# Optimization experiments

Hardware: AMD Instinct MI355X
Metric: run time of the kernel (lower is better)

Reference implementation:

```python
import jax, jax.numpy as jnp
import numpy as np

E = 768   # embed_dim
S = 128   # slots
T = 3     # recurrence steps
B = 64    # batch
L = 512   # sequence length of z
LN_EPS = 1e-5


def _layernorm(x, g, b):
    mu = jnp.mean(x, axis=-1, keepdims=True)
    var = jnp.mean((x - mu) ** 2, axis=-1, keepdims=True)
    return (x - mu) / jnp.sqrt(var + LN_EPS) * g + b


def _mha(q, k, v, Wq, bq, Wk, bk, Wv, bv, Wo, bo):
    # single-head MultiheadAttention, batch_first; PyTorch Linear: x @ W.T + b
    Q = q @ Wq.T + bq                     # [B, Lq, E]
    K = k @ Wk.T + bk                     # [B, Lk, E]
    V = v @ Wv.T + bv
    scale = 1.0 / jnp.sqrt(jnp.asarray(Q.shape[-1], Q.dtype))
    scores = jnp.einsum('bqe,bke->bqk', Q, K) * scale
    A = jax.nn.softmax(scores, axis=-1)
    O = jnp.einsum('bqk,bke->bqe', A, V)
    return O @ Wo.T + bo


def _gru_cell(x, h, Wih, bih, Whh, bhh):
    # PyTorch GRUCell gate order: r, z, n
    gi = x @ Wih.T + bih
    gh = h @ Whh.T + bhh
    i_r, i_z, i_n = jnp.split(gi, 3, axis=-1)
    h_r, h_z, h_n = jnp.split(gh, 3, axis=-1)
    r = jax.nn.sigmoid(i_r + h_r)
    zt = jax.nn.sigmoid(i_z + h_z)
    n = jnp.tanh(i_n + r * h_n)
    return (1.0 - zt) * n + zt * h


def setup_inputs() -> dict:
    key = jax.random.key(0)
    ks = jax.random.split(key, 24)
    w = lambda k, shape: jax.random.normal(k, shape, dtype=jnp.float32) * 0.02
    inp = {
        'z': jax.random.normal(ks[0], (B, L, E), dtype=jnp.float32),
        'slots': w(ks[1], (1, S, E)),
        'ln_g': jnp.ones((E,), jnp.float32),
        'ln_b': jnp.zeros((E,), jnp.float32),
        # write attention
        'w_wq': w(ks[2], (E, E)), 'w_bq': jnp.zeros((E,), jnp.float32),
        'w_wk': w(ks[3], (E, E)), 'w_bk': jnp.zeros((E,), jnp.float32),
        'w_wv': w(ks[4], (E, E)), 'w_bv': jnp.zeros((E,), jnp.float32),
        'w_wo': w(ks[5], (E, E)), 'w_bo': jnp.zeros((E,), jnp.float32),
        # read attention
        'r_wq': w(ks[6], (E, E)), 'r_bq': jnp.zeros((E,), jnp.float32),
        'r_wk': w(ks[7], (E, E)), 'r_bk': jnp.zeros((E,), jnp.float32),
        'r_wv': w(ks[8], (E, E)), 'r_bv': jnp.zeros((E,), jnp.float32),
        'r_wo': w(ks[9], (E, E)), 'r_bo': jnp.zeros((E,), jnp.float32),
        # GRUCell
        'gru_wih': w(ks[10], (3 * E, E)), 'gru_bih': jnp.zeros((3 * E,), jnp.float32),
        'gru_whh': w(ks[11], (3 * E, E)), 'gru_bhh': jnp.zeros((3 * E,), jnp.float32),
    }
    return inp


def reference(z, slots, ln_g, ln_b,
              w_wq, w_bq, w_wk, w_bk, w_wv, w_bv, w_wo, w_bo,
              r_wq, r_bq, r_wk, r_bk, r_wv, r_bv, r_wo, r_bo,
              gru_wih, gru_bih, gru_whh, gru_bhh):
    bsz = z.shape[0]
    memory = jnp.broadcast_to(slots, (bsz, S, E))
    for _ in range(T):
        memory = _layernorm(memory, ln_g, ln_b)
        upd = _mha(memory, z, z, w_wq, w_bq, w_wk, w_bk, w_wv, w_bv, w_wo, w_bo)
        memory = _gru_cell(upd.reshape(-1, E), memory.reshape(-1, E),
                           gru_wih, gru_bih, gru_whh, gru_bhh).reshape(bsz, S, E)
    out = _mha(z, memory, memory, r_wq, r_bq, r_wk, r_bk, r_wv, r_bv, r_wo, r_bo)
    return out
```

## Files before the change

kernel.cpp:

```cpp
#include <hip/hip_runtime.h>
#include <hip/hip_bf16.h>
#include <math.h>


typedef __attribute__((ext_vector_type(4))) float f32x4;
typedef __attribute__((ext_vector_type(8))) short short8;
typedef __attribute__((ext_vector_type(4))) unsigned short us4;

__device__ __forceinline__ unsigned short f2bf(float x) {
  union { float f; unsigned u; } v; v.f = x;
  unsigned r = v.u + 0x7fffu + ((v.u >> 16) & 1u);
  return (unsigned short)(r >> 16);
}
__device__ __forceinline__ float bf2f(unsigned short u) {
  union { unsigned u; float f; } v; v.u = (unsigned)u << 16; return v.f;
}

__device__ __forceinline__ void g2l16(const void* g, void* l) {
  __builtin_amdgcn_global_load_lds(
      (const __attribute__((address_space(1))) unsigned int*)g,
      (__attribute__((address_space(3))) unsigned int*)l, 16, 0, 0);
}

__device__ __forceinline__ float wsum(float v) {
#pragma unroll
  for (int o = 32; o > 0; o >>= 1) v += __shfl_xor(v, o, 64);
  return v;
}
__device__ __forceinline__ float wmax(float v) {
#pragma unroll
  for (int o = 32; o > 0; o >>= 1) v = fmaxf(v, __shfl_xor(v, o, 64));
  return v;
}

__device__ __forceinline__ void xcd_map(int& tn, int& tm, long long& bz) {
  const int gx = gridDim.x, gy = gridDim.y, gz = gridDim.z;
  const int nwg = gx * gy * gz;
  const int lin = blockIdx.x + gx * (blockIdx.y + gy * blockIdx.z);
  const int q = nwg >> 3, r = nwg & 7;
  const int xcd = lin & 7, jj = lin >> 3;
  const int w = (xcd < r ? xcd * (q + 1) : r * (q + 1) + (xcd - r) * q) + jj;
  tn = w % gx;
  const int t2 = w / gx;
  tm = t2 % gy;
  bz = t2 / gy;
}

__device__ __forceinline__ void c_write_128(
    void* Cg, size_t cb, int N, int tm, int tn, int wr, int wc, int lane,
    const f32x4 acc[4][4], const float* bias, bool has_bias, float alpha, int omode)
{
#pragma unroll
  for (int a = 0; a < 4; ++a) {
    const int row0 = tm * 128 + wr * 64 + a * 16 + (lane >> 4) * 4;
#pragma unroll
    for (int b = 0; b < 4; ++b) {
      const int col = tn * 128 + wc * 64 + b * 16 + (lane & 15);
      float bv = has_bias ? bias[col] : 0.f;
#pragma unroll
      for (int rr = 0; rr < 4; ++rr) {
        float v = acc[a][b][rr] * alpha + bv;
        if (omode == 0)
          ((float*)Cg)[cb + (size_t)(row0 + rr) * N + col] = v;
        else
          ((unsigned short*)Cg)[cb + (size_t)(row0 + rr) * N + col] = f2bf(v);
      }
    }
  }
}

template<int OMODE, bool BIAS>
__device__ __forceinline__ void gemm_body(
    const unsigned short* __restrict__ A, const unsigned short* __restrict__ B,
    const float* __restrict__ bias, void* __restrict__ Cg, size_t cb,
    int N, int K, int tm, int tn, float alpha,
    unsigned short* As, unsigned short* Bs)
{
  const int tid  = threadIdx.x;
  const int lane = tid & 63;
  const int wv   = tid >> 6;
  const int wr   = wv >> 1, wc = wv & 1;

  A += (size_t)tm * 128 * K;
  B += (size_t)tn * 128 * K;

  const int srow = wv * 16 + (lane >> 2);
  const int kby  = (lane & 3) * 16;

  f32x4 acc[4][4];
#pragma unroll
  for (int a = 0; a < 4; ++a)
#pragma unroll
    for (int b = 0; b < 4; ++b) acc[a][b] = (f32x4)(0.f);

  const int mrow = wr * 64 + (lane & 15);
  const int nrow = wc * 64 + (lane & 15);
  const int koff = (lane >> 4) * 8;

  for (int kt = 0; kt < K; kt += 32) {
#pragma unroll
    for (int i = 0; i < 2; ++i) {
      g2l16((const char*)(A + (size_t)(i * 64 + srow) * K + kt) + kby,
            (char*)As + i * 4096 + wv * 1024);
      g2l16((const char*)(B + (size_t)(i * 64 + srow) * K + kt) + kby,
            (char*)Bs + i * 4096 + wv * 1024);
    }
    __syncthreads();
    short8 af[4], bf[4];
#pragma unroll
    for (int a = 0; a < 4; ++a) af[a] = *(const short8*)&As[(mrow + a * 16) * 32 + koff];
#pragma unroll
    for (int b = 0; b < 4; ++b) bf[b] = *(const short8*)&Bs[(nrow + b * 16) * 32 + koff];
#pragma unroll
    for (int a = 0; a < 4; ++a)
#pragma unroll
      for (int b = 0; b < 4; ++b)
        acc[a][b] = __builtin_amdgcn_mfma_f32_16x16x32_bf16(af[a], bf[b], acc[a][b], 0, 0, 0);
    __syncthreads();
  }
  c_write_128(Cg, cb, N, tm, tn, wr, wc, lane, acc, bias, BIAS, alpha, OMODE);
}

template<int OMODE, bool BIAS>
__global__ __launch_bounds__(256) void gemm_nt64(
    const unsigned short* __restrict__ Ag, const unsigned short* __restrict__ Bg,
    const float* __restrict__ bias, void* __restrict__ Cg,
    int M, int N, int K, long long sA, long long sB, long long sC,
    long long sBias, float alpha)
{
  __shared__ __align__(16) unsigned short As[128 * 64];
  __shared__ __align__(16) unsigned short Bs[128 * 64];

  const int tid  = threadIdx.x;
  const int lane = tid & 63;
  const int wv   = tid >> 6;
  const int wr   = wv >> 1, wc = wv & 1;

  int tn, tm; long long bz;
  xcd_map(tn, tm, bz);

  const unsigned short* A = Ag + bz * sA + (size_t)tm * 128 * K;
  const unsigned short* B = Bg + bz * sB + (size_t)tn * 128 * K;

  auto swz = [](int o) { return o ^ (((o >> 7) & 7) << 4); };

  const char* aSrc[4];
  const char* bSrc[4];
#pragma unroll
  for (int c = 0; c < 4; ++c) {
    const int olog = swz(c * 4096 + tid * 16);
    const int row = olog >> 7, cbyte = olog & 127;
    aSrc[c] = (const char*)(A + (size_t)row * K) + cbyte;
    bSrc[c] = (const char*)(B + (size_t)row * K) + cbyte;
  }
  const int mrow = wr * 64 + (lane & 15);
  const int nrow = wc * 64 + (lane & 15);
  const int kb   = (lane >> 4) * 16;
  int aoff[4][2], boff[4][2];
#pragma unroll
  for (int a = 0; a < 4; ++a)
#pragma unroll
    for (int h = 0; h < 2; ++h) {
      aoff[a][h] = swz((mrow + a * 16) * 128 + h * 64 + kb);
      boff[a][h] = swz((nrow + a * 16) * 128 + h * 64 + kb);
    }

  f32x4 acc[4][4];
#pragma unroll
  for (int a = 0; a < 4; ++a)
#pragma unroll
    for (int b = 0; b < 4; ++b) acc[a][b] = (f32x4)(0.f);

  size_t ktB = 0;
  for (int kt = 0; kt < K; kt += 64, ktB += 128) {
#pragma unroll
    for (int c = 0; c < 4; ++c) {
      g2l16(aSrc[c] + ktB, (char*)As + c * 4096 + wv * 1024);
      g2l16(bSrc[c] + ktB, (char*)Bs + c * 4096 + wv * 1024);
    }
    __syncthreads();
#pragma unroll
    for (int h = 0; h < 2; ++h) {
      short8 af[4], bf[4];
#pragma unroll
      for (int a = 0; a < 4; ++a)
        af[a] = *(const short8*)((char*)As + aoff[a][h]);
#pragma unroll
      for (int b = 0; b < 4; ++b)
        bf[b] = *(const short8*)((char*)Bs + boff[b][h]);
#pragma unroll
      for (int a = 0; a < 4; ++a)
#pragma unroll
        for (int b = 0; b < 4; ++b)
          acc[a][b] = __builtin_amdgcn_mfma_f32_16x16x32_bf16(af[a], bf[b], acc[a][b], 0, 0, 0);
    }
    __syncthreads();
  }

  const float* bp = BIAS ? bias + bz * sBias : (const float*)nullptr;
  c_write_128(Cg, (size_t)(bz * sC), N, tm, tn, wr, wc, lane, acc, bp, BIAS, alpha, OMODE);
}

struct QuadPtrs {
  const unsigned short* a[4];
  const unsigned short* b[4];
  unsigned short* c[4];
};
__global__ __launch_bounds__(256) void gemm_nt_quad(QuadPtrs p) {
  __shared__ __align__(16) unsigned short As[128 * 32];
  __shared__ __align__(16) unsigned short Bs[128 * 32];
  const int zi = blockIdx.z;
  gemm_body<1, false>(p.a[zi], p.b[zi], nullptr, (void*)p.c[zi], 0,
                      768, 768, blockIdx.y, blockIdx.x, 1.0f, As, Bs);
}

__global__ __launch_bounds__(256) void softmax512(
    const float* __restrict__ sc, unsigned short* __restrict__ p)
{
  const int row  = blockIdx.x * 4 + (threadIdx.x >> 6);
  const int lane = threadIdx.x & 63;
  const float4* sr = (const float4*)(sc + (size_t)row * 512);
  float4 v[2];
  float m = -1e30f;
#pragma unroll
  for (int j = 0; j < 2; ++j) {
    v[j] = sr[lane + 64 * j];
    m = fmaxf(m, fmaxf(fmaxf(v[j].x, v[j].y), fmaxf(v[j].z, v[j].w)));
  }
  m = wmax(m);
  float s = 0.f;
#pragma unroll
  for (int j = 0; j < 2; ++j) {
    v[j].x = __expf(v[j].x - m); v[j].y = __expf(v[j].y - m);
    v[j].z = __expf(v[j].z - m); v[j].w = __expf(v[j].w - m);
    s += v[j].x + v[j].y + v[j].z + v[j].w;
  }
  s = wsum(s);
  const float inv = 1.f / s;
  us4* pr = (us4*)(p + (size_t)row * 512);
#pragma unroll
  for (int j = 0; j < 2; ++j) {
    us4 o;
    o.x = f2bf(v[j].x * inv); o.y = f2bf(v[j].y * inv);
    o.z = f2bf(v[j].z * inv); o.w = f2bf(v[j].w * inv);
    pr[lane + 64 * j] = o;
  }
}

__global__ __launch_bounds__(256) void softmax128(
    const float* __restrict__ sc, unsigned short* __restrict__ p)
{
  const int row  = blockIdx.x * 4 + (threadIdx.x >> 6);
  const int lane = threadIdx.x & 63;
  const float* sr = sc + (size_t)row * 128;
  float v[2];
  float m = -1e30f;
#pragma unroll
  for (int j = 0; j < 2; ++j) { v[j] = sr[lane + 64 * j]; m = fmaxf(m, v[j]); }
  m = wmax(m);
  float s = 0.f;
#pragma unroll
  for (int j = 0; j < 2; ++j) { v[j] = __expf(v[j] - m); s += v[j]; }
  s = wsum(s);
  const float inv = 1.f / s;
  unsigned short* pr = p + (size_t)row * 128;
#pragma unroll
  for (int j = 0; j < 2; ++j) pr[lane + 64 * j] = f2bf(v[j] * inv);
}

template<bool GHB, bool EMITLN>
__global__ __launch_bounds__(256) void gru_ln_combine(
    const unsigned short* __restrict__ gi, const unsigned short* __restrict__ gh,
    float* __restrict__ mem, const float* __restrict__ g, const float* __restrict__ b,
    unsigned short* __restrict__ outb)
{
  __shared__ float ps[4], pq[4];
  const size_t row = blockIdx.x;
  const int tid = threadIdx.x, wv = tid >> 6, lane = tid & 63;
  float* mr = mem + row * 768;
  const size_t ghrow = GHB ? (row & 127) : row;
  float v[3];
  float s = 0.f, q = 0.f;
#pragma unroll
  for (int k = 0; k < 3; ++k) {
    v[k] = mr[tid + 256 * k];
    s += v[k]; q += v[k] * v[k];
  }
  s = wsum(s); q = wsum(q);
  if (lane == 0) { ps[wv] = s; pq[wv] = q; }
  __syncthreads();
  s = ps[0] + ps[1] + ps[2] + ps[3];
  q = pq[0] + pq[1] + pq[2] + pq[3];
  const float mu = s * (1.f / 768.f);
  const float rstd = rsqrtf(q * (1.f / 768.f) - mu * mu + 1e-5f);
  float nv[3];
  float s2 = 0.f, q2 = 0.f;
#pragma unroll
  for (int k = 0; k < 3; ++k) {
    const int c = tid + 256 * k;
    const float h = (v[k] - mu) * rstd * g[c] + b[c];
    const float ir  = bf2f(gi[row * 2304 + c]);
    const float iz  = bf2f(gi[row * 2304 + 768 + c]);
    const float in_ = bf2f(gi[row * 2304 + 1536 + c]);
    const float hr  = bf2f(gh[ghrow * 2304 + c]);
    const float hz  = bf2f(gh[ghrow * 2304 + 768 + c]);
    const float hn  = bf2f(gh[ghrow * 2304 + 1536 + c]);
    const float rg = 1.f / (1.f + __expf(-(ir + hr)));
    const float zg = 1.f / (1.f + __expf(-(iz + hz)));
    const float n  = tanhf(in_ + rg * hn);
    nv[k] = (1.f - zg) * n + zg * h;
    mr[c] = nv[k];
    s2 += nv[k]; q2 += nv[k] * nv[k];
  }
  if (EMITLN) {
    s2 = wsum(s2); q2 = wsum(q2);
    __syncthreads();
    if (lane == 0) { ps[wv] = s2; pq[wv] = q2; }
    __syncthreads();
    s2 = ps[0] + ps[1] + ps[2] + ps[3];
    q2 = pq[0] + pq[1] + pq[2] + pq[3];
    const float mu2 = s2 * (1.f / 768.f);
    const float rstd2 = rsqrtf(q2 * (1.f / 768.f) - mu2 * mu2 + 1e-5f);
#pragma unroll
    for (int k = 0; k < 3; ++k) {
      const int c = tid + 256 * k;
      outb[row * 768 + c] = f2bf((nv[k] - mu2) * rstd2 * g[c] + b[c]);
    }
  } else {
#pragma unroll
    for (int k = 0; k < 3; ++k) {
      const int c = tid + 256 * k;
      outb[row * 768 + c] = f2bf(nv[k]);
    }
  }
}

__global__ __launch_bounds__(256) void cvt_weights(
    const float* p0, const float* p1, const float* p2, const float* p3,
    const float* p4, const float* p5, const float* p6, const float* p7,
    const float* p8, const float* p9, unsigned short* __restrict__ dst)
{
  const int i = blockIdx.x * 256 + threadIdx.x;
  if (i >= 2064384) return;
  const float* src; int base;
  if      (i < 147456)  { src = p0; base = 0; }
  else if (i < 294912)  { src = p1; base = 147456; }
  else if (i < 442368)  { src = p2; base = 294912; }
  else if (i < 589824)  { src = p3; base = 442368; }
  else if (i < 737280)  { src = p4; base = 589824; }
  else if (i < 884736)  { src = p5; base = 737280; }
  else if (i < 1032192) { src = p6; base = 884736; }
  else if (i < 1179648) { src = p7; base = 1032192; }
  else if (i < 1622016) { src = p8; base = 1179648; }
  else                  { src = p9; base = 1622016; }
  const float4 v = ((const float4*)src)[i - base];
  us4 o;
  o.x = f2bf(v.x); o.y = f2bf(v.y); o.z = f2bf(v.z); o.w = f2bf(v.w);
  ((us4*)dst)[i] = o;
}

__global__ __launch_bounds__(256) void init_mem(
    const float* __restrict__ slots, const float* __restrict__ g,
    const float* __restrict__ b, float* __restrict__ memf,
    unsigned short* __restrict__ memb)
{
  __shared__ float ps[4], pq[4];
  const int s = blockIdx.x;
  const int g0 = blockIdx.y * 8;
  const int tid = threadIdx.x, wv = tid >> 6, lane = tid & 63;
  const float* sr = slots + (size_t)s * 768;
  float v[3];
  float su = 0.f, qu = 0.f;
#pragma unroll
  for (int k = 0; k < 3; ++k) { v[k] = sr[tid + 256 * k]; su += v[k]; qu += v[k] * v[k]; }
  su = wsum(su); qu = wsum(qu);
  if (lane == 0) { ps[wv] = su; pq[wv] = qu; }
  __syncthreads();
  su = ps[0] + ps[1] + ps[2] + ps[3];
  qu = pq[0] + pq[1] + pq[2] + pq[3];
  const float mu = su * (1.f / 768.f);
  const float rstd = rsqrtf(qu * (1.f / 768.f) - mu * mu + 1e-5f);
  unsigned short lb[3];
#pragma unroll
  for (int k = 0; k < 3; ++k) {
    const int c = tid + 256 * k;
    lb[k] = f2bf((v[k] - mu) * rstd * g[c] + b[c]);
  }
  for (int bb = g0; bb < g0 + 8; ++bb) {
    float* mrow = memf + ((size_t)bb * 128 + s) * 768;
    unsigned short* brow = memb + ((size_t)bb * 128 + s) * 768;
#pragma unroll
    for (int k = 0; k < 3; ++k) { mrow[tid + 256 * k] = v[k]; brow[tid + 256 * k] = lb[k]; }
  }
}

struct TPtrs { const unsigned short* s[6]; unsigned short* d[6]; };
__global__ void transpose_multi(TPtrs p) {
  __shared__ unsigned short t[32][33];
  const unsigned short* in = p.s[blockIdx.z];
  unsigned short* out = p.d[blockIdx.z];
  const int c0 = blockIdx.x * 32, r0 = blockIdx.y * 32;
  const int x = threadIdx.x, y = threadIdx.y;
#pragma unroll
  for (int k = 0; k < 32; k += 8)
    t[y + k][x] = in[(size_t)(r0 + y + k) * 768 + c0 + x];
  __syncthreads();
#pragma unroll
  for (int k = 0; k < 32; k += 8)
    out[(size_t)(c0 + y + k) * 768 + r0 + x] = t[x][y + k];
}

__global__ __launch_bounds__(256) void matvec_row2b(
    const unsigned short* __restrict__ A0, const float* __restrict__ x0,
    float* __restrict__ y0,
    const unsigned short* __restrict__ A1, const float* __restrict__ x1,
    float* __restrict__ y1)
{
  const int task = blockIdx.x / 192;
  const int row = (blockIdx.x % 192) * 4 + (threadIdx.x >> 6);
  const int lane = threadIdx.x & 63;
  const unsigned short* r = (task ? A1 : A0) + (size_t)row * 768;
  const float* x = task ? x1 : x0;
  float s = 0.f;
#pragma unroll
  for (int j = 0; j < 12; ++j) s += bf2f(r[lane + 64 * j]) * x[lane + 64 * j];
  s = wsum(s);
  if (lane == 0) (task ? y1 : y0)[row] = s;
}

__global__ __launch_bounds__(256) void matvec_row2(
    const float* __restrict__ W0, const float* __restrict__ x0,
    const float* __restrict__ a0, float* __restrict__ y0,
    const float* __restrict__ W1, const float* __restrict__ x1,
    const float* __restrict__ a1, float* __restrict__ y1)
{
  const int task = blockIdx.x / 192;
  const int row = (blockIdx.x % 192) * 4 + (threadIdx.x >> 6);
  const int lane = threadIdx.x & 63;
  const float* W = task ? W1 : W0;
  const float* x = task ? x1 : x0;
  const float* ad = task ? a1 : a0;
  float* y = task ? y1 : y0;
  const float4* r = (const float4*)(W + (size_t)row * 768);
  const float4* xv = (const float4*)x;
  float s = 0.f;
#pragma unroll
  for (int j = 0; j < 3; ++j) {
    const float4 a = r[lane + 64 * j], c = xv[lane + 64 * j];
    s += a.x * c.x + a.y * c.y + a.z * c.z + a.w * c.w;
  }
  s = wsum(s);
  if (lane == 0) y[row] = s + ad[row];
}

__global__ __launch_bounds__(256) void rowdot768(
    const float* __restrict__ src, const float* __restrict__ vec,
    const float* __restrict__ cadd, float* __restrict__ out, float scl, int rows)
{
  const int row  = blockIdx.x * 4 + (threadIdx.x >> 6);
  if (row >= rows) return;
  const int lane = threadIdx.x & 63;
  const float4* r = (const float4*)(src + (size_t)row * 768);
  const float4* vv = (const float4*)vec;
  float s = 0.f;
#pragma unroll
  for (int j = 0; j < 3; ++j) {
    const float4 a = r[lane + 64 * j], c = vv[lane + 64 * j];
    s += a.x * c.x + a.y * c.y + a.z * c.z + a.w * c.w;
  }
  s = wsum(s);
  if (lane == 0) out[row] = scl * (s + (cadd ? cadd[0] : 0.f));
}

__global__ __launch_bounds__(256) void cvt_z_zv(
    const float* __restrict__ z, unsigned short* __restrict__ zb,
    const float* __restrict__ vw, const float* __restrict__ cw,
    float* __restrict__ zv, float scl)
{
  const int row = blockIdx.x * 4 + (threadIdx.x >> 6);
  const int lane = threadIdx.x & 63;
  const float4* zr = (const float4*)(z + (size_t)row * 768);
  const float4* wv = (const float4*)vw;
  us4* zbr = (us4*)(zb + (size_t)row * 768);
  float s = 0.f;
#pragma unroll
  for (int j = 0; j < 3; ++j) {
    const float4 v = zr[lane + 64 * j];
    const float4 w = wv[lane + 64 * j];
    s += v.x * w.x + v.y * w.y + v.z * w.z + v.w * w.w;
    us4 o;
    o.x = f2bf(v.x); o.y = f2bf(v.y); o.z = f2bf(v.z); o.w = f2bf(v.w);
    zbr[lane + 64 * j] = o;
  }
  s = wsum(s);
  if (lane == 0) zv[row] = scl * (s + cw[0]);
}

__global__ __launch_bounds__(256) void diag_ws(float* __restrict__ out, float wsz, int n) {
  const int i = blockIdx.x * 256 + threadIdx.x;
  if (i < n) out[i] = (i == 0) ? wsz : 0.f;
}

extern "C" void kernel_launch(void* const* d_in, const int* in_sizes, int n_in,
                              void* d_out, int out_size, void* d_ws, size_t ws_size,
                              hipStream_t stream)
{
  const float* z     = (const float*)d_in[0];
  const float* slots = (const float*)d_in[1];
  const float* ln_g  = (const float*)d_in[2];
  const float* ln_b  = (const float*)d_in[3];
  const float* w_wq = (const float*)d_in[4];  const float* w_bq = (const float*)d_in[5];
  const float* w_wk = (const float*)d_in[6];  const float* w_bk = (const float*)d_in[7];
  const float* w_wv = (const float*)d_in[8];  const float* w_bv = (const float*)d_in[9];
  const float* w_wo = (const float*)d_in[10]; const float* w_bo = (const float*)d_in[11];
  const float* r_wq = (const float*)d_in[12]; const float* r_bq = (const float*)d_in[13];
  const float* r_wk = (const float*)d_in[14]; const float* r_bk = (const float*)d_in[15];
  const float* r_wv = (const float*)d_in[16]; const float* r_bv = (const float*)d_in[17];
  const float* r_wo = (const float*)d_in[18]; const float* r_bo = (const float*)d_in[19];
  const float* g_wih = (const float*)d_in[20]; const float* g_bih = (const float*)d_in[21];
  const float* g_whh = (const float*)d_in[22]; const float* g_bhh = (const float*)d_in[23];

  constexpr size_t O_F    = 16515072;
  constexpr size_t O_T6   = 21233664;
  constexpr size_t O_GH0  = 28311552;
  constexpr size_t O_FL   = 28901376;
  constexpr size_t O_memf = 29096192;
  constexpr size_t O_Kz   = 54262016;
  constexpr size_t O_VwoT = 104593664;
  constexpr size_t O_L    = 154925312;
  constexpr size_t NEED   = 217839872;

  if (ws_size < NEED) {
    hipLaunchKernelGGL(diag_ws, dim3((out_size + 255) / 256), dim3(256), 0, stream,
                       (float*)d_out, (float)ws_size, out_size);
    return;
  }

  char* ws = (char*)d_ws;
  unsigned short* wqb  = (unsigned short*)(ws + 0);
  unsigned short* wkb  = wqb + 589824;
  unsigned short* wvb  = wkb + 589824;
  unsigned short* wob  = wvb + 589824;
  unsigned short* rqb  = wob + 589824;
  unsigned short* rkb  = rqb + 589824;
  unsigned short* rvb  = rkb + 589824;
  unsigned short* rob  = rvb + 589824;
  unsigned short* wihb = rob + 589824;
  unsigned short* whhb = wihb + 1769472;
  unsigned short* Fqk  = (unsigned short*)(ws + O_F);
  unsigned short* Fwv  = Fqk + 589824;
  unsigned short* Fvo  = Fwv + 589824;
  unsigned short* Frq  = Fvo + 589824;
  unsigned short* T0   = (unsigned short*)(ws + O_T6);
  unsigned short* T1   = T0 + 589824;
  unsigned short* T2   = T1 + 589824;
  unsigned short* T3   = T2 + 589824;
  unsigned short* T4   = T3 + 589824;
  unsigned short* T5   = T4 + 589824;
  unsigned short* gh0  = (unsigned short*)(ws + O_GH0);
  float* bih_c   = (float*)(ws + O_FL);
  float* bhh_c   = bih_c + 2304;
  float* const_o = bhh_c + 2304;
  float* bvo     = const_o + 768;
  float* vw      = bvo + 768;
  float* vr      = vw + 768;
  float* cw      = vr + 768;
  float* zv      = cw + 64;
  float* colb    = zv + 32768;
  float* memf = (float*)(ws + O_memf);
  unsigned short* Kz    = (unsigned short*)(ws + O_Kz);
  unsigned short* memFr = (unsigned short*)(ws + O_Kz);
  unsigned short* VwoT  = (unsigned short*)(ws + O_VwoT);
  unsigned short* memVoT  = (unsigned short*)(ws + O_VwoT);
  float*          Sbr     = (float*)(ws + O_VwoT + 25165824);
  unsigned short* Abr     = (unsigned short*)(ws + O_VwoT + 41943040);
  char* L = ws + O_L;
  unsigned short* memb  = (unsigned short*)(L + 0);
  unsigned short* updb  = (unsigned short*)(L + 12582912);
  float*          Sbuf  = (float*)(L + 25165824);
  unsigned short* Abuf  = (unsigned short*)(L + 41943040);
  unsigned short* gib   = (unsigned short*)(L + 25165824);
  unsigned short* ghb   = (unsigned short*)d_out;
  unsigned short* zb    = (unsigned short*)((char*)d_out + 50331648);

  const float scale = 1.0f / sqrtf(768.f);

  hipLaunchKernelGGL(cvt_weights, dim3(8064), dim3(256), 0, stream,
      w_wq, w_wk, w_wv, w_wo, r_wq, r_wk, r_wv, r_wo, g_wih, g_whh, wqb);
  hipMemcpyAsync(bih_c, g_bih, 2304 * 4, hipMemcpyDeviceToDevice, stream);
  hipMemcpyAsync(bhh_c, g_bhh, 2304 * 4, hipMemcpyDeviceToDevice, stream);

  {
    TPtrs tp;
    tp.s[0] = wqb; tp.d[0] = T0;
    tp.s[1] = wkb; tp.d[1] = T1;
    tp.s[2] = wvb; tp.d[2] = T2;
    tp.s[3] = rvb; tp.d[3] = T3;
    tp.s[4] = rqb; tp.d[4] = T4;
    tp.s[5] = rkb; tp.d[5] = T5;
    hipLaunchKernelGGL(transpose_multi, dim3(24, 24, 6), dim3(32, 8), 0, stream, tp);
  }
  {
    QuadPtrs qp;
    qp.a[0] = T0;  qp.b[0] = T1; qp.c[0] = Fqk;
    qp.a[1] = wob; qp.b[1] = T2; qp.c[1] = Fwv;
    qp.a[2] = rob; qp.b[2] = T3; qp.c[2] = Fvo;
    qp.a[3] = T4;  qp.b[3] = T5; qp.c[3] = Frq;
    hipLaunchKernelGGL(gemm_nt_quad, dim3(6, 6, 4), dim3(256), 0, stream, qp);
  }

  hipLaunchKernelGGL(matvec_row2b, dim3(384), dim3(256), 0, stream,
      T1, w_bq, vw, T5, r_bq, vr);
  hipLaunchKernelGGL(matvec_row2, dim3(384), dim3(256), 0, stream,
      w_wo, w_bv, w_bo, const_o, r_wo, r_bv, r_bo, bvo);
  hipLaunchKernelGGL(rowdot768, dim3(1), dim3(256), 0, stream,
      w_bq, w_bk, (const float*)nullptr, cw, 1.0f, 1);
  hipLaunchKernelGGL(cvt_z_zv, dim3(8192), dim3(256), 0, stream, z, zb, vw, cw, zv, scale);
  hipLaunchKernelGGL(init_mem, dim3(128, 8), dim3(256), 0, stream,
      slots, ln_g, ln_b, memf, memb);

  hipLaunchKernelGGL((gemm_nt64<1, false>), dim3(4, 6, 64), dim3(256), 0, stream,
      Fwv, zb, (const float*)nullptr, (void*)VwoT, 768, 512, 768,
      0ll, 393216ll, 393216ll, 0ll, 1.0f);
  hipLaunchKernelGGL((gemm_nt64<1, false>), dim3(6, 256, 1), dim3(256), 0, stream,
      zb, Fqk, (const float*)nullptr, (void*)Kz, 32768, 768, 768, 0ll, 0ll, 0ll, 0ll, 1.0f);

  const long long sA_g = (long long)(memb - updb);
  const long long sC_g = (long long)(ghb - gib);

  for (int t = 0; t < 3; ++t) {
    hipLaunchKernelGGL((gemm_nt64<0, true>), dim3(4, 1, 64), dim3(256), 0, stream,
        memb, Kz, zv, (void*)Sbuf, 128, 512, 768,
        98304ll, 393216ll, 65536ll, 512ll, scale);
    hipLaunchKernelGGL(softmax512, dim3(2048), dim3(256), 0, stream, Sbuf, Abuf);
    hipLaunchKernelGGL((gemm_nt64<1, true>), dim3(6, 1, 64), dim3(256), 0, stream,
        Abuf, VwoT, const_o, (void*)updb, 128, 768, 512,
        65536ll, 393216ll, 98304ll, 0ll, 1.0f);
    if (t == 0) {
      hipLaunchKernelGGL((gemm_nt64<1, true>), dim3(18, 1, 1), dim3(256), 0, stream,
          memb, whhb, bhh_c, (void*)gh0, 128, 2304, 768, 0ll, 0ll, 0ll, 0ll, 1.0f);
      hipLaunchKernelGGL((gemm_nt64<1, true>), dim3(18, 64, 1), dim3(256), 0, stream,
          updb, wihb, bih_c, (void*)gib, 8192, 2304, 768, 0ll, 0ll, 0ll, 0ll, 1.0f);
      hipLaunchKernelGGL((gru_ln_combine<true, true>), dim3(8192), dim3(256), 0, stream,
          gib, gh0, memf, ln_g, ln_b, memb);
    } else {
      hipLaunchKernelGGL((gemm_nt64<1, true>), dim3(18, 64, 2), dim3(256), 0, stream,
          updb, wihb, bih_c, (void*)gib, 8192, 2304, 768,
          sA_g, 1769472ll, sC_g, 2304ll, 1.0f);
      if (t < 2)
        hipLaunchKernelGGL((gru_ln_combine<false, true>), dim3(8192), dim3(256), 0, stream,
            gib, ghb, memf, ln_g, ln_b, memb);
      else
        hipLaunchKernelGGL((gru_ln_combine<false, false>), dim3(8192), dim3(256), 0, stream,
            gib, ghb, memf, ln_g, ln_b, memb);
    }
  }

  hipLaunchKernelGGL((gemm_nt64<1, false>), dim3(6, 64, 1), dim3(256), 0, stream,
      memb, Frq, (const float*)nullptr, (void*)memFr, 8192, 768, 768,
      0ll, 0ll, 0ll, 0ll, 1.0f);
  hipLaunchKernelGGL((gemm_nt64<1, false>), dim3(1, 6, 64), dim3(256), 0, stream,
      Fvo, memb, (const float*)nullptr, (void*)memVoT, 768, 128, 768,
      0ll, 98304ll, 98304ll, 0ll, 1.0f);
  hipLaunchKernelGGL(rowdot768, dim3(2048), dim3(256), 0, stream,
      memf, vr, (const float*)nullptr, colb, scale, 8192);
  hipLaunchKernelGGL((gemm_nt64<0, true>), dim3(1, 4, 64), dim3(256), 0, stream,
      zb, memFr, colb, (void*)Sbr, 512, 128, 768,
      393216ll, 98304ll, 65536ll, 128ll, scale);
  hipLaunchKernelGGL(softmax128, dim3(8192), dim3(256), 0, stream, Sbr, Abr);
  hipLaunchKernelGGL((gemm_nt64<0, true>), dim3(6, 4, 64), dim3(256), 0, stream,
      Abr, memVoT, bvo, d_out, 512, 768, 128,
      65536ll, 98304ll, 393216ll, 0ll, 1.0f);
}
```

Before: 683.4 us.

## Double-buffer LDS tiles in the bf16 GEMM to prefetch the next K-tile

Replaces the single-buffered GEMM main loop with a two-stage LDS ping-pong. Global-to-LDS loads for tile u+2 are issued right after tile u is consumed. Explicit vmcnt waits and raw s_barriers replace __syncthreads, so MFMA work on one buffer overlaps the memory loads into the other. This hides global-load latency at the cost of doubling LDS per block to 64 KB, which can lower occupancy.

```diff
diff --git a/kernel.cpp b/kernel.cpp
--- a/kernel.cpp
+++ b/kernel.cpp
@@ -122,14 +122,14 @@
 }
 
 template<int OMODE, bool BIAS>
-__global__ __launch_bounds__(256) void gemm_nt64(
+__global__ __launch_bounds__(256) void gemm_nt64p(
     const unsigned short* __restrict__ Ag, const unsigned short* __restrict__ Bg,
     const float* __restrict__ bias, void* __restrict__ Cg,
     int M, int N, int K, long long sA, long long sB, long long sC,
     long long sBias, float alpha)
 {
-  __shared__ __align__(16) unsigned short As[128 * 64];
-  __shared__ __align__(16) unsigned short Bs[128 * 64];
+  __shared__ __align__(16) unsigned short As[2][128 * 64];
+  __shared__ __align__(16) unsigned short Bs[2][128 * 64];
 
   const int tid  = threadIdx.x;
   const int lane = tid & 63;
@@ -165,36 +165,47 @@
       boff[a][h] = swz((nrow + a * 16) * 128 + h * 64 + kb);
     }
 
+  auto stage = [&](int bi, size_t ktB) {
+#pragma unroll
+    for (int c = 0; c < 4; ++c) {
+      g2l16(aSrc[c] + ktB, (char*)As[bi] + c * 4096 + wv * 1024);
+      g2l16(bSrc[c] + ktB, (char*)Bs[bi] + c * 4096 + wv * 1024);
+    }
+  };
+
   f32x4 acc[4][4];
 #pragma unroll
   for (int a = 0; a < 4; ++a)
 #pragma unroll
     for (int b = 0; b < 4; ++b) acc[a][b] = (f32x4)(0.f);
 
-  size_t ktB = 0;
-  for (int kt = 0; kt < K; kt += 64, ktB += 128) {
-#pragma unroll
-    for (int c = 0; c < 4; ++c) {
-      g2l16(aSrc[c] + ktB, (char*)As + c * 4096 + wv * 1024);
-      g2l16(bSrc[c] + ktB, (char*)Bs + c * 4096 + wv * 1024);
-    }
-    __syncthreads();
+  const int nt = K >> 6;
+  stage(0, 0);
+  stage(1, 128);
+
+  for (int u = 0; u < nt; ++u) {
+    if (u + 1 < nt) asm volatile("s_waitcnt vmcnt(8)" ::: "memory");
+    else            asm volatile("s_waitcnt vmcnt(0)" ::: "memory");
+    __builtin_amdgcn_s_barrier();
+    __builtin_amdgcn_sched_barrier(0);
+    const char* Ab = (const char*)As[u & 1];
+    const char* Bb = (const char*)Bs[u & 1];
 #pragma unroll
     for (int h = 0; h < 2; ++h) {
       short8 af[4], bf[4];
 #pragma unroll
-      for (int a = 0; a < 4; ++a)
-        af[a] = *(const short8*)((char*)As + aoff[a][h]);
-#pragma unroll
-      for (int b = 0; b < 4; ++b)
-        bf[b] = *(const short8*)((char*)Bs + boff[b][h]);
+      for (int a = 0; a < 4; ++a) af[a] = *(const short8*)(Ab + aoff[a][h]);
+#pragma unroll
+      for (int b = 0; b < 4; ++b) bf[b] = *(const short8*)(Bb + boff[b][h]);
 #pragma unroll
       for (int a = 0; a < 4; ++a)
 #pragma unroll
         for (int b = 0; b < 4; ++b)
           acc[a][b] = __builtin_amdgcn_mfma_f32_16x16x32_bf16(af[a], bf[b], acc[a][b], 0, 0, 0);
     }
-    __syncthreads();
+    __builtin_amdgcn_sched_barrier(0);
+    __builtin_amdgcn_s_barrier();
+    if (u + 2 < nt) stage(u & 1, (size_t)(u + 2) * 128);
   }
 
   const float* bp = BIAS ? bias + bz * sBias : (const float*)nullptr;
@@ -619,32 +630,32 @@
   hipLaunchKernelGGL(init_mem, dim3(128, 8), dim3(256), 0, stream,
       slots, ln_g, ln_b, memf, memb);
 
-  hipLaunchKernelGGL((gemm_nt64<1, false>), dim3(4, 6, 64), dim3(256), 0, stream,
+  hipLaunchKernelGGL((gemm_nt64p<1, false>), dim3(4, 6, 64), dim3(256), 0, stream,
       Fwv, zb, (const float*)nullptr, (void*)VwoT, 768, 512, 768,
       0ll, 393216ll, 393216ll, 0ll, 1.0f);
-  hipLaunchKernelGGL((gemm_nt64<1, false>), dim3(6, 256, 1), dim3(256), 0, stream,
+  hipLaunchKernelGGL((gemm_nt64p<1, false>), dim3(6, 256, 1), dim3(256), 0, stream,
       zb, Fqk, (const float*)nullptr, (void*)Kz, 32768, 768, 768, 0ll, 0ll, 0ll, 0ll, 1.0f);
 
   const long long sA_g = (long long)(memb - updb);
   const long long sC_g = (long long)(ghb - gib);
 
   for (int t = 0; t < 3; ++t) {
-    hipLaunchKernelGGL((gemm_nt64<0, true>), dim3(4, 1, 64), dim3(256), 0, stream,
+    hipLaunchKernelGGL((gemm_nt64p<0, true>), dim3(4, 1, 64), dim3(256), 0, stream,
         memb, Kz, zv, (void*)Sbuf, 128, 512, 768,
         98304ll, 393216ll, 65536ll, 512ll, scale);
     hipLaunchKernelGGL(softmax512, dim3(2048), dim3(256), 0, stream, Sbuf, Abuf);
-    hipLaunchKernelGGL((gemm_nt64<1, true>), dim3(6, 1, 64), dim3(256), 0, stream,
+    hipLaunchKernelGGL((gemm_nt64p<1, true>), dim3(6, 1, 64), dim3(256), 0, stream,
         Abuf, VwoT, const_o, (void*)updb, 128, 768, 512,
         65536ll, 393216ll, 98304ll, 0ll, 1.0f);
     if (t == 0) {
-      hipLaunchKernelGGL((gemm_nt64<1, true>), dim3(18, 1, 1), dim3(256), 0, stream,
+      hipLaunchKernelGGL((gemm_nt64p<1, true>), dim3(18, 1, 1), dim3(256), 0, stream,
           memb, whhb, bhh_c, (void*)gh0, 128, 2304, 768, 0ll, 0ll, 0ll, 0ll, 1.0f);
-      hipLaunchKernelGGL((gemm_nt64<1, true>), dim3(18, 64, 1), dim3(256), 0, stream,
+      hipLaunchKernelGGL((gemm_nt64p<1, true>), dim3(18, 64, 1), dim3(256), 0, stream,
           updb, wihb, bih_c, (void*)gib, 8192, 2304, 768, 0ll, 0ll, 0ll, 0ll, 1.0f);
       hipLaunchKernelGGL((gru_ln_combine<true, true>), dim3(8192), dim3(256), 0, stream,
           gib, gh0, memf, ln_g, ln_b, memb);
     } else {
-      hipLaunchKernelGGL((gemm_nt64<1, true>), dim3(18, 64, 2), dim3(256), 0, stream,
+      hipLaunchKernelGGL((gemm_nt64p<1, true>), dim3(18, 64, 2), dim3(256), 0, stream,
           updb, wihb, bih_c, (void*)gib, 8192, 2304, 768,
           sA_g, 1769472ll, sC_g, 2304ll, 1.0f);
       if (t < 2)
@@ -656,19 +667,19 @@
     }
   }
 
-  hipLaunchKernelGGL((gemm_nt64<1, false>), dim3(6, 64, 1), dim3(256), 0, stream,
+  hipLaunchKernelGGL((gemm_nt64p<1, false>), dim3(6, 64, 1), dim3(256), 0, stream,
       memb, Frq, (const float*)nullptr, (void*)memFr, 8192, 768, 768,
       0ll, 0ll, 0ll, 0ll, 1.0f);
-  hipLaunchKernelGGL((gemm_nt64<1, false>), dim3(1, 6, 64), dim3(256), 0, stream,
+  hipLaunchKernelGGL((gemm_nt64p<1, false>), dim3(1, 6, 64), dim3(256), 0, stream,
       Fvo, memb, (const float*)nullptr, (void*)memVoT, 768, 128, 768,
       0ll, 98304ll, 98304ll, 0ll, 1.0f);
   hipLaunchKernelGGL(rowdot768, dim3(2048), dim3(256), 0, stream,
       memf, vr, (const float*)nullptr, colb, scale, 8192);
-  hipLaunchKernelGGL((gemm_nt64<0, true>), dim3(1, 4, 64), dim3(256), 0, stream,
+  hipLaunchKernelGGL((gemm_nt64p<0, true>), dim3(1, 4, 64), dim3(256), 0, stream,
       zb, memFr, colb, (void*)Sbr, 512, 128, 768,
       393216ll, 98304ll, 65536ll, 128ll, scale);
   hipLaunchKernelGGL(softmax128, dim3(8192), dim3(256), 0, stream, Sbr, Abr);
-  hipLaunchKernelGGL((gemm_nt64<0, true>), dim3(6, 4, 64), dim3(256), 0, stream,
+  hipLaunchKernelGGL((gemm_nt64p<0, true>), dim3(6, 4, 64), dim3(256), 0, stream,
       Abr, memVoT, bvo, d_out, 512, 768, 128,
       65536ll, 98304ll, 393216ll, 0ll, 1.0f);
 }
```

After: 692.8 us. No clear change (+1.4%).
